# Optimization experiments

Measured on AMD Instinct MI355X. Metric: run time of the kernel, lower is better.

Reference implementation:

```python
import jax, jax.numpy as jnp
import numpy as np

N = 262144
H = 256
R = 32


def setup_inputs() -> dict:
    key = jax.random.key(0)
    ks = jax.random.split(key, 16)
    s = 1.0 / np.sqrt(H)
    return {
        "x": jax.random.normal(ks[0], (N, 1), jnp.float32),
        "t": jax.random.uniform(ks[1], (N, 1), jnp.float32),
        "start_w": jax.random.normal(ks[2], (H, 2), jnp.float32) * 0.5,
        "start_b": jax.random.normal(ks[3], (H,), jnp.float32) * 0.1,
        "end_w": jax.random.normal(ks[4], (1, H), jnp.float32) * s,
        "end_b": jax.random.normal(ks[5], (1,), jnp.float32) * 0.1,
        "col_0": jax.random.normal(ks[6], (H, R), jnp.float32) * s,
        "col_1": jax.random.normal(ks[7], (H, R), jnp.float32) * s,
        "col_2": jax.random.normal(ks[8], (H, R), jnp.float32) * s,
        "row_0": jax.random.normal(ks[9], (H, R), jnp.float32) * s,
        "row_1": jax.random.normal(ks[10], (H, R), jnp.float32) * s,
        "row_2": jax.random.normal(ks[11], (H, R), jnp.float32) * s,
        "alpha_0": jax.random.normal(ks[12], (R,), jnp.float32),
        "alpha_1": jax.random.normal(ks[13], (R,), jnp.float32),
        "alpha_2": jax.random.normal(ks[14], (R,), jnp.float32),
    }


def reference(x, t, start_w, start_b, end_w, end_b,
              col_0, col_1, col_2, row_0, row_1, row_2,
              alpha_0, alpha_1, alpha_2):
    # inputs: [N,2] -> start Linear -> tanh
    inp = jnp.concatenate([x, t], axis=1)
    h = jnp.tanh(inp @ start_w.T + start_b)  # [N, H]
    # three low-rank blocks: h @ (col * diag(alpha)) @ row.T, then tanh.
    # col_basis @ diag(alpha) == col_basis * alpha[None, :] (column scaling)
    for col, row, alpha in ((col_0, row_0, alpha_0),
                            (col_1, row_1, alpha_1),
                            (col_2, row_2, alpha_2)):
        h = jnp.tanh((h @ (col * alpha)) @ row.T)  # [N,H]->[N,R]->[N,H]
    return h @ end_w.T + end_b  # [N, 1]
```

## Files before the change

### kernel.cpp

```cpp
#include <hip/hip_runtime.h>


typedef _Float16 half4_t __attribute__((ext_vector_type(4)));
typedef float    float4_t __attribute__((ext_vector_type(4)));

namespace {

struct Smem {
  half4_t ctf[3 * 16 * 2 * 64];
  half4_t rwf[3 * 16 * 2 * 64];
  float w0[256], w1[256], bb[256], ew[256];
};

__device__ __forceinline__ float fast_tanh(float x) {
  float e = __builtin_amdgcn_exp2f(x * 2.885390081777927f);
  return 1.0f - 2.0f * __builtin_amdgcn_rcpf(e + 1.0f);
}

__device__ __forceinline__ half4_t tanh4_pack(float4_t v) {
  half4_t h;
  h.x = (_Float16)fast_tanh(v.x);
  h.y = (_Float16)fast_tanh(v.y);
  h.z = (_Float16)fast_tanh(v.z);
  h.w = (_Float16)fast_tanh(v.w);
  return h;
}

__global__ __launch_bounds__(1024) void pinn_fused(
    const float* __restrict__ xg, const float* __restrict__ tg,
    const float* __restrict__ sw, const float* __restrict__ sb,
    const float* __restrict__ ewp, const float* __restrict__ ebp,
    const float* __restrict__ c0, const float* __restrict__ c1,
    const float* __restrict__ c2, const float* __restrict__ r0,
    const float* __restrict__ r1, const float* __restrict__ r2,
    const float* __restrict__ a0, const float* __restrict__ a1,
    const float* __restrict__ a2, float* __restrict__ out, int n)
{
  __shared__ Smem sm;
  const int tid = threadIdx.x;

  for (int e = tid; e < 3 * 16 * 2 * 64; e += 1024) {
    const int lane_ = e & 63;
    const int sel   = (e >> 6) & 1;
    const int t_    = (e >> 7) & 15;
    const int k_    = e >> 11;
    const int m_ = lane_ & 15, q_ = lane_ >> 4;
    const float* ck = (k_ == 0) ? c0 : (k_ == 1) ? c1 : c2;
    const float* rk = (k_ == 0) ? r0 : (k_ == 1) ? r1 : r2;
    const float* ak = (k_ == 0) ? a0 : (k_ == 1) ? a1 : a2;
    {
      const int r = sel * 16 + m_;
      const float av = ak[r];
      const int j0 = 16 * t_ + 4 * q_;
      half4_t v;
      v.x = (_Float16)(ck[(j0 + 0) * 32 + r] * av);
      v.y = (_Float16)(ck[(j0 + 1) * 32 + r] * av);
      v.z = (_Float16)(ck[(j0 + 2) * 32 + r] * av);
      v.w = (_Float16)(ck[(j0 + 3) * 32 + r] * av);
      sm.ctf[e] = v;
    }
    {
      const int j = 16 * t_ + m_;
      const int rr = sel * 16 + 4 * q_;
      half4_t v;
      v.x = (_Float16)rk[j * 32 + rr + 0];
      v.y = (_Float16)rk[j * 32 + rr + 1];
      v.z = (_Float16)rk[j * 32 + rr + 2];
      v.w = (_Float16)rk[j * 32 + rr + 3];
      sm.rwf[e] = v;
    }
  }
  if (tid < 256) {
    sm.w0[tid] = sw[2 * tid];
    sm.w1[tid] = sw[2 * tid + 1];
    sm.bb[tid] = sb[tid];
    sm.ew[tid] = ewp[tid];
  }
  __syncthreads();

  const int wave = tid >> 6;
  const int lane = tid & 63;
  const int m = lane & 15;
  const int q = lane >> 4;
  const int wo = 4 * q;
  const float ebv = ebp[0];
  const int tiles = n >> 4;

#pragma unroll 1
  for (int g = blockIdx.x * 16 + wave; g < tiles; g += 4096) {
    const int n0 = g * 16;
    const float xm = xg[n0 + m];
    const float tm = tg[n0 + m];

    float4_t acc0 = {0.f, 0.f, 0.f, 0.f};
    float4_t acc1 = {0.f, 0.f, 0.f, 0.f};
#pragma unroll 1
    for (int t = 0; t < 16; ++t) {
      const int cb = t * 16 + wo;
      const float4_t w0v = *(const float4_t*)&sm.w0[cb];
      const float4_t w1v = *(const float4_t*)&sm.w1[cb];
      const float4_t bv  = *(const float4_t*)&sm.bb[cb];
      float4_t z;
      z.x = fmaf(xm, w0v.x, fmaf(tm, w1v.x, bv.x));
      z.y = fmaf(xm, w0v.y, fmaf(tm, w1v.y, bv.y));
      z.z = fmaf(xm, w0v.z, fmaf(tm, w1v.z, bv.z));
      z.w = fmaf(xm, w0v.w, fmaf(tm, w1v.w, bv.w));
      const half4_t h = tanh4_pack(z);
      const half4_t* cp = &sm.ctf[t * 128 + lane];
      acc0 = __builtin_amdgcn_mfma_f32_16x16x16f16(cp[0], h, acc0, 0, 0, 0);
      acc1 = __builtin_amdgcn_mfma_f32_16x16x16f16(cp[64], h, acc1, 0, 0, 0);
    }

    float ssum = 0.0f;
#pragma unroll 1
    for (int k = 0; k < 3; ++k) {
      const half4_t pfA = {(_Float16)acc0.x, (_Float16)acc0.y, (_Float16)acc0.z, (_Float16)acc0.w};
      const half4_t pfB = {(_Float16)acc1.x, (_Float16)acc1.y, (_Float16)acc1.z, (_Float16)acc1.w};

      if (k < 2) {
        float4_t na = {0.f, 0.f, 0.f, 0.f};
        float4_t nb = {0.f, 0.f, 0.f, 0.f};
        const half4_t* rp = &sm.rwf[k * 2048 + lane];
        const half4_t* cp = &sm.ctf[(k + 1) * 2048 + lane];
#pragma unroll 1
        for (int t = 0; t < 16; ++t) {
          float4_t hc = {0.f, 0.f, 0.f, 0.f};
          hc = __builtin_amdgcn_mfma_f32_16x16x16f16(rp[0], pfA, hc, 0, 0, 0);
          hc = __builtin_amdgcn_mfma_f32_16x16x16f16(rp[64], pfB, hc, 0, 0, 0);
          const half4_t h = tanh4_pack(hc);
          na = __builtin_amdgcn_mfma_f32_16x16x16f16(cp[0], h, na, 0, 0, 0);
          nb = __builtin_amdgcn_mfma_f32_16x16x16f16(cp[64], h, nb, 0, 0, 0);
          rp += 128;
          cp += 128;
        }
        acc0 = na;
        acc1 = nb;
      } else {
        const half4_t* rp = &sm.rwf[2 * 2048 + lane];
#pragma unroll 1
        for (int t = 0; t < 16; ++t) {
          float4_t hc = {0.f, 0.f, 0.f, 0.f};
          hc = __builtin_amdgcn_mfma_f32_16x16x16f16(rp[0], pfA, hc, 0, 0, 0);
          hc = __builtin_amdgcn_mfma_f32_16x16x16f16(rp[64], pfB, hc, 0, 0, 0);
          const float4_t ev = *(const float4_t*)&sm.ew[t * 16 + wo];
          ssum += fast_tanh(hc.x) * ev.x + fast_tanh(hc.y) * ev.y
                + fast_tanh(hc.z) * ev.z + fast_tanh(hc.w) * ev.w;
          rp += 128;
        }
      }
    }
    ssum += __shfl_xor(ssum, 16);
    ssum += __shfl_xor(ssum, 32);
    if (lane < 16) out[n0 + m] = ssum + ebv;
  }
}

}

extern "C" void kernel_launch(void* const* d_in, const int* in_sizes, int n_in,
                              void* d_out, int out_size, void* d_ws, size_t ws_size,
                              hipStream_t stream) {
  const float* xg  = (const float*)d_in[0];
  const float* tg  = (const float*)d_in[1];
  const float* sw  = (const float*)d_in[2];
  const float* sb  = (const float*)d_in[3];
  const float* ewp = (const float*)d_in[4];
  const float* ebp = (const float*)d_in[5];
  const float* c0  = (const float*)d_in[6];
  const float* c1  = (const float*)d_in[7];
  const float* c2  = (const float*)d_in[8];
  const float* r0  = (const float*)d_in[9];
  const float* r1  = (const float*)d_in[10];
  const float* r2  = (const float*)d_in[11];
  const float* a0  = (const float*)d_in[12];
  const float* a1  = (const float*)d_in[13];
  const float* a2  = (const float*)d_in[14];
  float* outp = (float*)d_out;

  const int n = in_sizes[0];

  pinn_fused<<<256, 1024, 0, stream>>>(xg, tg, sw, sb, ewp, ebp,
                                       c0, c1, c2, r0, r1, r2, a0, a1, a2,
                                       outp, n);
}
```

Measured before the change: 162.1 us.

## Process four row tiles per wave and fold tanh scale into weights

Each wave now handles four 16-row tiles at once, so every LDS load of the col/row basis fragments feeds four independent MFMAs. This amortizes shared-memory traffic and gives the scheduler independent MFMA chains to hide latency. The 2/ln2 tanh prescale is folded into the start weights and row bases, and fp16 packing uses cvt_pkrtz. It raises register pressure, and pkrtz rounds toward zero, which slightly changes numerics.

```diff
diff --git a/kernel.cpp b/kernel.cpp
--- a/kernel.cpp
+++ b/kernel.cpp
@@ -2,31 +2,43 @@
 
 
 typedef _Float16 half4_t __attribute__((ext_vector_type(4)));
+typedef __fp16   fp16x2  __attribute__((ext_vector_type(2)));
 typedef float    float4_t __attribute__((ext_vector_type(4)));
 
+#define TANH_SCALE 2.885390081777927f
+#define MFMA16 __builtin_amdgcn_mfma_f32_16x16x16f16
+
 namespace {
 
-struct Smem {
+struct alignas(16) Smem {
   half4_t ctf[3 * 16 * 2 * 64];
   half4_t rwf[3 * 16 * 2 * 64];
-  float w0[256], w1[256], bb[256], ew[256];
+  float w0[256], w1[256], bb[256];
+  float ew[256];
 };
 
-__device__ __forceinline__ float fast_tanh(float x) {
-  float e = __builtin_amdgcn_exp2f(x * 2.885390081777927f);
-  return 1.0f - 2.0f * __builtin_amdgcn_rcpf(e + 1.0f);
-}
-
-__device__ __forceinline__ half4_t tanh4_pack(float4_t v) {
-  half4_t h;
-  h.x = (_Float16)fast_tanh(v.x);
-  h.y = (_Float16)fast_tanh(v.y);
-  h.z = (_Float16)fast_tanh(v.z);
-  h.w = (_Float16)fast_tanh(v.w);
-  return h;
-}
-
-__global__ __launch_bounds__(1024) void pinn_fused(
+__device__ __forceinline__ half4_t pack4(float4_t v) {
+  union { fp16x2 f2[2]; half4_t h4; } u;
+  u.f2[0] = __builtin_amdgcn_cvt_pkrtz(v.x, v.y);
+  u.f2[1] = __builtin_amdgcn_cvt_pkrtz(v.z, v.w);
+  return u.h4;
+}
+
+__device__ __forceinline__ float tanh_pre(float y) {
+  const float e = __builtin_amdgcn_exp2f(y);
+  return fmaf(-2.0f, __builtin_amdgcn_rcpf(e + 1.0f), 1.0f);
+}
+
+__device__ __forceinline__ half4_t tanh4(float4_t v) {
+  float4_t r;
+  r.x = tanh_pre(v.x); r.y = tanh_pre(v.y);
+  r.z = tanh_pre(v.z); r.w = tanh_pre(v.w);
+  return pack4(r);
+}
+
+__global__ __launch_bounds__(1024)
+__attribute__((amdgpu_waves_per_eu(4, 4)))
+void pinn_fused(
     const float* __restrict__ xg, const float* __restrict__ tg,
     const float* __restrict__ sw, const float* __restrict__ sb,
     const float* __restrict__ ewp, const float* __restrict__ ebp,
@@ -63,17 +75,17 @@
       const int j = 16 * t_ + m_;
       const int rr = sel * 16 + 4 * q_;
       half4_t v;
-      v.x = (_Float16)rk[j * 32 + rr + 0];
-      v.y = (_Float16)rk[j * 32 + rr + 1];
-      v.z = (_Float16)rk[j * 32 + rr + 2];
-      v.w = (_Float16)rk[j * 32 + rr + 3];
+      v.x = (_Float16)(rk[j * 32 + rr + 0] * TANH_SCALE);
+      v.y = (_Float16)(rk[j * 32 + rr + 1] * TANH_SCALE);
+      v.z = (_Float16)(rk[j * 32 + rr + 2] * TANH_SCALE);
+      v.w = (_Float16)(rk[j * 32 + rr + 3] * TANH_SCALE);
       sm.rwf[e] = v;
     }
   }
   if (tid < 256) {
-    sm.w0[tid] = sw[2 * tid];
-    sm.w1[tid] = sw[2 * tid + 1];
-    sm.bb[tid] = sb[tid];
+    sm.w0[tid] = sw[2 * tid] * TANH_SCALE;
+    sm.w1[tid] = sw[2 * tid + 1] * TANH_SCALE;
+    sm.bb[tid] = sb[tid] * TANH_SCALE;
     sm.ew[tid] = ewp[tid];
   }
   __syncthreads();
@@ -86,72 +98,118 @@
   const float ebv = ebp[0];
   const int tiles = n >> 4;
 
-#pragma unroll 1
-  for (int g = blockIdx.x * 16 + wave; g < tiles; g += 4096) {
-    const int n0 = g * 16;
-    const float xm = xg[n0 + m];
-    const float tm = tg[n0 + m];
-
-    float4_t acc0 = {0.f, 0.f, 0.f, 0.f};
-    float4_t acc1 = {0.f, 0.f, 0.f, 0.f};
+  const float4_t z4 = {0.f, 0.f, 0.f, 0.f};
+
+#pragma unroll 1
+  for (int g = (blockIdx.x * 16 + wave) * 4; g < tiles; g += 16384) {
+    float xm[4], tm[4];
+#pragma unroll
+    for (int s = 0; s < 4; ++s) {
+      xm[s] = xg[(g + s) * 16 + m];
+      tm[s] = tg[(g + s) * 16 + m];
+    }
+
+    float4_t acc[4][2];
+#pragma unroll
+    for (int s = 0; s < 4; ++s) { acc[s][0] = z4; acc[s][1] = z4; }
+    const half4_t* cp0 = &sm.ctf[lane];
 #pragma unroll 1
     for (int t = 0; t < 16; ++t) {
       const int cb = t * 16 + wo;
       const float4_t w0v = *(const float4_t*)&sm.w0[cb];
       const float4_t w1v = *(const float4_t*)&sm.w1[cb];
       const float4_t bv  = *(const float4_t*)&sm.bb[cb];
-      float4_t z;
-      z.x = fmaf(xm, w0v.x, fmaf(tm, w1v.x, bv.x));
-      z.y = fmaf(xm, w0v.y, fmaf(tm, w1v.y, bv.y));
-      z.z = fmaf(xm, w0v.z, fmaf(tm, w1v.z, bv.z));
-      z.w = fmaf(xm, w0v.w, fmaf(tm, w1v.w, bv.w));
-      const half4_t h = tanh4_pack(z);
-      const half4_t* cp = &sm.ctf[t * 128 + lane];
-      acc0 = __builtin_amdgcn_mfma_f32_16x16x16f16(cp[0], h, acc0, 0, 0, 0);
-      acc1 = __builtin_amdgcn_mfma_f32_16x16x16f16(cp[64], h, acc1, 0, 0, 0);
-    }
-
-    float ssum = 0.0f;
-#pragma unroll 1
-    for (int k = 0; k < 3; ++k) {
-      const half4_t pfA = {(_Float16)acc0.x, (_Float16)acc0.y, (_Float16)acc0.z, (_Float16)acc0.w};
-      const half4_t pfB = {(_Float16)acc1.x, (_Float16)acc1.y, (_Float16)acc1.z, (_Float16)acc1.w};
-
-      if (k < 2) {
-        float4_t na = {0.f, 0.f, 0.f, 0.f};
-        float4_t nb = {0.f, 0.f, 0.f, 0.f};
-        const half4_t* rp = &sm.rwf[k * 2048 + lane];
-        const half4_t* cp = &sm.ctf[(k + 1) * 2048 + lane];
-#pragma unroll 1
-        for (int t = 0; t < 16; ++t) {
-          float4_t hc = {0.f, 0.f, 0.f, 0.f};
-          hc = __builtin_amdgcn_mfma_f32_16x16x16f16(rp[0], pfA, hc, 0, 0, 0);
-          hc = __builtin_amdgcn_mfma_f32_16x16x16f16(rp[64], pfB, hc, 0, 0, 0);
-          const half4_t h = tanh4_pack(hc);
-          na = __builtin_amdgcn_mfma_f32_16x16x16f16(cp[0], h, na, 0, 0, 0);
-          nb = __builtin_amdgcn_mfma_f32_16x16x16f16(cp[64], h, nb, 0, 0, 0);
-          rp += 128;
-          cp += 128;
+      half4_t h[4];
+#pragma unroll
+      for (int s = 0; s < 4; ++s) {
+        float4_t z;
+        z.x = fmaf(xm[s], w0v.x, fmaf(tm[s], w1v.x, bv.x));
+        z.y = fmaf(xm[s], w0v.y, fmaf(tm[s], w1v.y, bv.y));
+        z.z = fmaf(xm[s], w0v.z, fmaf(tm[s], w1v.z, bv.z));
+        z.w = fmaf(xm[s], w0v.w, fmaf(tm[s], w1v.w, bv.w));
+        h[s] = tanh4(z);
+      }
+      const half4_t cA = cp0[0], cB = cp0[64];
+#pragma unroll
+      for (int s = 0; s < 4; ++s) acc[s][0] = MFMA16(cA, h[s], acc[s][0], 0, 0, 0);
+#pragma unroll
+      for (int s = 0; s < 4; ++s) acc[s][1] = MFMA16(cB, h[s], acc[s][1], 0, 0, 0);
+      cp0 += 128;
+    }
+
+#pragma unroll 1
+    for (int k = 0; k < 2; ++k) {
+      half4_t pf[4][2];
+#pragma unroll
+      for (int s = 0; s < 4; ++s) {
+        pf[s][0] = pack4(acc[s][0]);
+        pf[s][1] = pack4(acc[s][1]);
+      }
+      float4_t nn[4][2];
+#pragma unroll
+      for (int s = 0; s < 4; ++s) { nn[s][0] = z4; nn[s][1] = z4; }
+      const half4_t* rp = &sm.rwf[k * 2048 + lane];
+      const half4_t* cp = &sm.ctf[(k + 1) * 2048 + lane];
+#pragma unroll 1
+      for (int t = 0; t < 16; ++t) {
+        const half4_t rA = rp[0], rB = rp[64];
+        const half4_t cA = cp[0], cB = cp[64];
+        float4_t u[4];
+#pragma unroll
+        for (int s = 0; s < 4; ++s) u[s] = MFMA16(rA, pf[s][0], z4, 0, 0, 0);
+#pragma unroll
+        for (int s = 0; s < 4; ++s) u[s] = MFMA16(rB, pf[s][1], u[s], 0, 0, 0);
+        half4_t h[4];
+#pragma unroll
+        for (int s = 0; s < 4; ++s) h[s] = tanh4(u[s]);
+#pragma unroll
+        for (int s = 0; s < 4; ++s) nn[s][0] = MFMA16(cA, h[s], nn[s][0], 0, 0, 0);
+#pragma unroll
+        for (int s = 0; s < 4; ++s) nn[s][1] = MFMA16(cB, h[s], nn[s][1], 0, 0, 0);
+        rp += 128; cp += 128;
+      }
+#pragma unroll
+      for (int s = 0; s < 4; ++s) { acc[s][0] = nn[s][0]; acc[s][1] = nn[s][1]; }
+    }
+
+    float ssum[4] = {0.f, 0.f, 0.f, 0.f};
+    {
+      half4_t pf[4][2];
+#pragma unroll
+      for (int s = 0; s < 4; ++s) {
+        pf[s][0] = pack4(acc[s][0]);
+        pf[s][1] = pack4(acc[s][1]);
+      }
+      const half4_t* rp = &sm.rwf[2 * 2048 + lane];
+#pragma unroll 1
+      for (int t = 0; t < 16; ++t) {
+        const half4_t rA = rp[0], rB = rp[64];
+        const float4_t ev = *(const float4_t*)&sm.ew[t * 16 + wo];
+        float4_t u[4];
+#pragma unroll
+        for (int s = 0; s < 4; ++s) u[s] = MFMA16(rA, pf[s][0], z4, 0, 0, 0);
+#pragma unroll
+        for (int s = 0; s < 4; ++s) u[s] = MFMA16(rB, pf[s][1], u[s], 0, 0, 0);
+#pragma unroll
+        for (int s = 0; s < 4; ++s) {
+          ssum[s] = fmaf(ev.x, tanh_pre(u[s].x), ssum[s]);
+          ssum[s] = fmaf(ev.y, tanh_pre(u[s].y), ssum[s]);
+          ssum[s] = fmaf(ev.z, tanh_pre(u[s].z), ssum[s]);
+          ssum[s] = fmaf(ev.w, tanh_pre(u[s].w), ssum[s]);
         }
-        acc0 = na;
-        acc1 = nb;
-      } else {
-        const half4_t* rp = &sm.rwf[2 * 2048 + lane];
-#pragma unroll 1
-        for (int t = 0; t < 16; ++t) {
-          float4_t hc = {0.f, 0.f, 0.f, 0.f};
-          hc = __builtin_amdgcn_mfma_f32_16x16x16f16(rp[0], pfA, hc, 0, 0, 0);
-          hc = __builtin_amdgcn_mfma_f32_16x16x16f16(rp[64], pfB, hc, 0, 0, 0);
-          const float4_t ev = *(const float4_t*)&sm.ew[t * 16 + wo];
-          ssum += fast_tanh(hc.x) * ev.x + fast_tanh(hc.y) * ev.y
-                + fast_tanh(hc.z) * ev.z + fast_tanh(hc.w) * ev.w;
-          rp += 128;
-        }
-      }
-    }
-    ssum += __shfl_xor(ssum, 16);
-    ssum += __shfl_xor(ssum, 32);
-    if (lane < 16) out[n0 + m] = ssum + ebv;
+        rp += 128;
+      }
+    }
+
+#pragma unroll
+    for (int s = 0; s < 4; ++s) {
+      ssum[s] += __shfl_xor(ssum[s], 16);
+      ssum[s] += __shfl_xor(ssum[s], 32);
+    }
+    if (lane < 16) {
+#pragma unroll
+      for (int s = 0; s < 4; ++s) out[(g + s) * 16 + m] = ssum[s] + ebv;
+    }
   }
 }
 
```

After: 143.0 us. 1.13x faster.
